# Optimization experiments

Hardware: AMD Instinct MI355X
Metric: run time of the kernel (lower is better)

Reference implementation:

```python
import jax, jax.numpy as jnp
import numpy as np

N, E, H, EC, K, NH = 50000, 640000, 128, 64, 128, 4
Hh, Kh = H // NH, K // NH
LOG2 = float(np.log(2.0))

def ssp(x):
    # ShiftedSoftplus: softplus(x) - log(2)
    return jax.nn.softplus(x) - LOG2

def ln(x, g, b, eps=1e-5):
    m = jnp.mean(x, axis=-1, keepdims=True)
    v = jnp.var(x, axis=-1, keepdims=True)
    return (x - m) * jax.lax.rsqrt(v + eps) * g + b

def setup_inputs() -> dict:
    key = jax.random.key(0)
    ks = jax.random.split(key, 24)
    def nrm(k, shape, scale):
        return jax.random.normal(k, shape, jnp.float32) * scale
    s_h = 1.0 / np.sqrt(Hh); s_e = 1.0 / np.sqrt(EC); s_k = 1.0 / np.sqrt(Kh)
    inp = {}
    inp['x'] = nrm(ks[0], (N, H), 1.0)
    inp['edge_attr'] = nrm(ks[1], (E, EC), 1.0)
    inp['edge_index'] = jax.random.randint(ks[2], (2, E), 0, N)
    # grouped Conv1d(H,K,1,groups=NH) == per-head linear: weight (NH, Kh, Hh)
    inp['k_w'] = nrm(ks[3], (NH, Kh, Hh), s_h)
    inp['q_w'] = nrm(ks[4], (NH, Kh, Hh), s_h)
    inp['v_w'] = nrm(ks[5], (NH, Hh, Hh), s_h)
    inp['wk1_w'] = nrm(ks[6], (Kh, EC), s_e); inp['wk1_b'] = nrm(ks[7], (Kh,), 0.01)
    inp['wk2_w'] = nrm(ks[8], (Kh, Kh), s_k); inp['wk2_b'] = nrm(ks[9], (Kh,), 0.01)
    inp['wkl_w'] = nrm(ks[10], (Kh, Kh), s_k); inp['wkl_b'] = nrm(ks[11], (Kh,), 0.01)
    inp['wv1_w'] = nrm(ks[12], (Hh, EC), s_e); inp['wv1_b'] = nrm(ks[13], (Hh,), 0.01)
    inp['wv2_w'] = nrm(ks[14], (Hh, Hh), s_h); inp['wv2_b'] = nrm(ks[15], (Hh,), 0.01)
    inp['wvl_w'] = nrm(ks[16], (Hh, Hh), s_h); inp['wvl_b'] = nrm(ks[17], (Hh,), 0.01)
    inp['out_w'] = nrm(ks[18], (H, H), 1.0 / np.sqrt(H)); inp['out_b'] = nrm(ks[19], (H,), 0.01)
    inp['ln1_g'] = jnp.ones((H,), jnp.float32); inp['ln1_b'] = jnp.zeros((H,), jnp.float32)
    inp['ln2_g'] = jnp.ones((H,), jnp.float32); inp['ln2_b'] = jnp.zeros((H,), jnp.float32)
    return inp

def reference(x, edge_attr, k_w, q_w, v_w, wk1_w, wk1_b, wk2_w, wk2_b, wkl_w, wkl_b,
              wv1_w, wv1_b, wv2_w, wv2_b, wvl_w, wvl_b, out_w, out_b,
              ln1_g, ln1_b, ln2_g, ln2_b, edge_index):
    row, col = edge_index[0], edge_index[1]
    y = ln(x, ln1_g, ln1_b)
    yh = y.reshape(N, NH, Hh)
    h_k = jnp.einsum('nhd,hkd->nhk', yh, k_w)  # (N,NH,Kh)
    h_q = jnp.einsum('nhd,hkd->nhk', yh, q_w)
    h_v = jnp.einsum('nhd,hkd->nhk', yh, v_w)  # (N,NH,Hh)
    Wk = ssp(edge_attr @ wk1_w.T + wk1_b) @ wk2_w.T + wk2_b  # (E,Kh)
    keys_j = jnp.einsum('ehk,jk->ehj', Wk[:, None, :] * h_k[col], wkl_w) + wkl_b
    qk = jnp.sum(h_q[row] * keys_j, axis=-1)  # (E,NH)
    # scatter softmax over destination node `row`
    m = jax.ops.segment_max(qk, row, num_segments=N)
    ex = jnp.exp(qk - m[row])
    denom = jax.ops.segment_sum(ex, row, num_segments=N)
    alpha = ex / denom[row]  # (E,NH)
    Wv = ssp(edge_attr @ wv1_w.T + wv1_b) @ wv2_w.T + wv2_b  # (E,Hh)
    msg = jnp.einsum('ehd,jd->ehj', Wv[:, None, :] * h_v[col], wvl_w) + wvl_b
    msg = alpha[..., None] * msg  # (E,NH,Hh)
    aggr = jax.ops.segment_sum(msg, row, num_segments=N).reshape(N, H)
    x2 = aggr + x
    y2 = ln(x2, ln2_g, ln2_b)
    return ssp(y2) @ out_w.T + out_b + x2
```

## Files before the change

### kernel.cpp

```cpp
#include <hip/hip_runtime.h>
#include <math.h>

#define NN 50000
#define EE 640000
#define HD 128
#define ECD 64
#define NHD 4
#define HH 32
#define SCAN_B 256
#define NBLK ((NN + SCAN_B - 1) / SCAN_B)
#define LSTR 33
#define NTILE ((NN + 15) / 16)

typedef short bf16x8 __attribute__((ext_vector_type(8)));
typedef float f32x4 __attribute__((ext_vector_type(4)));

__device__ __forceinline__ float ssp_f(float v) {
    return fmaxf(v, 0.0f) + __logf(1.0f + __expf(-fabsf(v))) - 0.69314718055994531f;
}
__device__ __forceinline__ unsigned f2bf_u(float f) {
    unsigned u = __float_as_uint(f);
    unsigned r = ((u >> 16) & 1u) + 0x7FFFu;
    return (u + r) >> 16;
}
__device__ __forceinline__ unsigned pk2(float a, float b) {
    return f2bf_u(a) | (f2bf_u(b) << 16);
}
__device__ __forceinline__ unsigned f2bf_f(float f) {
    return (__float_as_uint(f) + 0x8000u) >> 16;
}
__device__ __forceinline__ unsigned pk2f(float a, float b) {
    return f2bf_f(a) | (f2bf_f(b) << 16);
}
__device__ __forceinline__ void unp2(unsigned u, float& a, float& b) {
    a = __uint_as_float(u << 16);
    b = __uint_as_float(u & 0xffff0000u);
}
__device__ __forceinline__ bf16x8 as_bf(uint4 u) {
    union { uint4 a; bf16x8 b; } c; c.a = u; return c.b;
}

__global__ __launch_bounds__(256) void k_ln1(
    const float* __restrict__ x, const float* __restrict__ ln1_g,
    const float* __restrict__ ln1_b, const float* __restrict__ cw,
    unsigned* __restrict__ y_bf, float* __restrict__ c0_out)
{
    const int w = threadIdx.x >> 6, l = threadIdx.x & 63;
    const int h = l >> 4, i16 = l & 15;
    const int t0 = 2 * l;
    const float2 lg2 = *(const float2*)(ln1_g + t0);
    const float2 lb2 = *(const float2*)(ln1_b + t0);
    const float2 cw2 = *(const float2*)(cw + t0);

    for (int n = blockIdx.x * 4 + w; n < NN; n += 2048 * 4) {
        const float2 xv = *(const float2*)(x + (size_t)n * HD + t0);
        float s1 = xv.x + xv.y;
        float s2 = xv.x * xv.x + xv.y * xv.y;
        #pragma unroll
        for (int off = 1; off < 64; off <<= 1) {
            s1 += __shfl_xor(s1, off);
            s2 += __shfl_xor(s2, off);
        }
        const float mean = s1 * (1.0f / HD);
        const float var  = s2 * (1.0f / HD) - mean * mean;
        const float rstd = rsqrtf(var + 1e-5f);
        const float y0 = (xv.x - mean) * rstd * lg2.x + lb2.x;
        const float y1 = (xv.y - mean) * rstd * lg2.y + lb2.y;
        y_bf[(size_t)n * 64 + l] = pk2(y0, y1);

        float p = y0 * cw2.x + y1 * cw2.y;
        #pragma unroll
        for (int off = 1; off < 16; off <<= 1) p += __shfl_xor(p, off);
        if (i16 == 0) c0_out[n * NHD + h] = p;
    }
}

__global__ __launch_bounds__(256) void k_pwfrag(
    const float* __restrict__ kw, const float* __restrict__ vw,
    const float* __restrict__ qw, const float* __restrict__ wklw,
    const float* __restrict__ wklb,
    uint4* __restrict__ pf, float* __restrict__ cw)
{
    const int t = threadIdx.x;
    #pragma unroll
    for (int it = 0; it < 6; ++it) {
        const int f = t + it * 256;
        const int tg = f >> 9;
        const int rem = f & 511;
        const int nt = rem >> 6, l = rem & 63;
        const int lm = l & 15, lg = l >> 4;
        const int h = nt >> 1, od = (nt & 1) * 16 + lm;
        float val[8];
        if (tg == 2) {
            #pragma unroll
            for (int j = 0; j < 8; ++j) {
                float s = 0.f;
                for (int j2 = 0; j2 < 32; ++j2)
                    s += qw[(size_t)(h * 32 + j2) * 32 + lg * 8 + j] * wklw[j2 * 32 + od];
                val[j] = s;
            }
        } else {
            const float* wp = (tg == 0) ? kw : vw;
            #pragma unroll
            for (int j = 0; j < 8; ++j)
                val[j] = wp[(size_t)(h * 32 + od) * 32 + lg * 8 + j];
        }
        uint4 o;
        o.x = pk2(val[0], val[1]); o.y = pk2(val[2], val[3]);
        o.z = pk2(val[4], val[5]); o.w = pk2(val[6], val[7]);
        pf[f] = o;
    }
    #pragma unroll
    for (int d2 = 0; d2 < 2; ++d2) {
        const int idx = t * 2 + d2;
        const int h = idx >> 5, d = idx & 31;
        float s = 0.f;
        for (int j = 0; j < 32; ++j)
            s += qw[(size_t)(h * 32 + j) * 32 + d] * wklb[j];
        cw[idx] = s;
    }
}

__global__ __launch_bounds__(256) void k_proj(
    const unsigned* __restrict__ y_bf, const uint4* __restrict__ pf,
    unsigned short* __restrict__ hk16, unsigned short* __restrict__ hv16,
    unsigned short* __restrict__ g16)
{
    const int w = threadIdx.x >> 6, l = threadIdx.x & 63;
    const int lm = l & 15, lg = l >> 4;
    const int tile = blockIdx.x * 4 + w;
    if (tile >= NTILE) return;
    const int n0 = tile * 16;

    uint4 af[4];
    #pragma unroll
    for (int h = 0; h < 4; ++h)
        af[h] = *(const uint4*)(y_bf + (size_t)(n0 + lm) * 64 + h * 16 + lg * 4);

    unsigned short* const outs[3] = {hk16, hv16, g16};
    #pragma unroll
    for (int tg = 0; tg < 3; ++tg) {
        f32x4 acc[8];
        #pragma unroll
        for (int nt = 0; nt < 8; ++nt) {
            acc[nt] = f32x4{0.f, 0.f, 0.f, 0.f};
            acc[nt] = __builtin_amdgcn_mfma_f32_16x16x32_bf16(
                as_bf(af[nt >> 1]), as_bf(pf[tg * 512 + nt * 64 + l]), acc[nt], 0, 0, 0);
        }
        unsigned short* o = outs[tg];
        #pragma unroll
        for (int nt = 0; nt < 8; ++nt)
            #pragma unroll
            for (int r = 0; r < 4; ++r)
                o[(size_t)(n0 + lg * 4 + r) * HD + nt * 16 + lm] =
                    (unsigned short)f2bf_u(acc[nt][r]);
    }
}

__global__ __launch_bounds__(256) void k_deg(
    const int* __restrict__ edge_index, int* __restrict__ deg)
{
    for (int e = blockIdx.x * blockDim.x + threadIdx.x; e < EE;
         e += gridDim.x * blockDim.x)
        atomicAdd(&deg[edge_index[e]], 1);
}

__global__ __launch_bounds__(SCAN_B) void k_scan_block(
    const int* __restrict__ deg, int* __restrict__ base, int* __restrict__ bsum)
{
    const int i = blockIdx.x * SCAN_B + threadIdx.x;
    const int v = (i < NN) ? deg[i] : 0;
    __shared__ int s[SCAN_B];
    s[threadIdx.x] = v;
    __syncthreads();
    for (int off = 1; off < SCAN_B; off <<= 1) {
        int t = (threadIdx.x >= off) ? s[threadIdx.x - off] : 0;
        __syncthreads();
        s[threadIdx.x] += t;
        __syncthreads();
    }
    if (i < NN) base[i] = s[threadIdx.x] - v;
    if (threadIdx.x == SCAN_B - 1) bsum[blockIdx.x] = s[SCAN_B - 1];
}

__global__ __launch_bounds__(SCAN_B) void k_scan_top(int* __restrict__ bsum)
{
    const int i = threadIdx.x;
    const int v = (i < NBLK) ? bsum[i] : 0;
    __shared__ int s[SCAN_B];
    s[i] = v;
    __syncthreads();
    for (int off = 1; off < SCAN_B; off <<= 1) {
        int t = (i >= off) ? s[i - off] : 0;
        __syncthreads();
        s[i] += t;
        __syncthreads();
    }
    if (i < NBLK) bsum[i] = s[i] - v;
}

__global__ __launch_bounds__(SCAN_B) void k_scan_add(
    int* __restrict__ base, const int* __restrict__ bsum, int* __restrict__ cursor)
{
    const int i = blockIdx.x * SCAN_B + threadIdx.x;
    if (i < NN) {
        const int b = base[i] + bsum[i >> 8];
        base[i] = b;
        cursor[i] = b;
    }
}

__global__ __launch_bounds__(256) void k_scatter(
    const int* __restrict__ edge_index, int* __restrict__ cursor,
    int* __restrict__ eidx, int* __restrict__ rowv, int* __restrict__ colv)
{
    for (int e = blockIdx.x * blockDim.x + threadIdx.x; e < EE;
         e += gridDim.x * blockDim.x) {
        const int r = edge_index[e];
        const int pos = atomicAdd(&cursor[r], 1);
        eidx[pos] = e;
        rowv[pos] = r;
        colv[pos] = edge_index[EE + e];
    }
}

__global__ __launch_bounds__(256) void k_ea_csr(
    const float* __restrict__ ea, const int* __restrict__ eidx,
    unsigned* __restrict__ ea_bf)
{
    for (int i = blockIdx.x * 256 + threadIdx.x; i < EE * 32;
         i += 2048 * 256) {
        const int pos = i >> 5, u = i & 31;
        const int e = eidx[pos];
        const float2 v = *(const float2*)(ea + (size_t)e * ECD + u * 2);
        ea_bf[(size_t)pos * 32 + u] = pk2(v.x, v.y);
    }
}

__global__ __launch_bounds__(256) void k_wfrag(
    const float* __restrict__ wk1_w, const float* __restrict__ wk2_w,
    const float* __restrict__ wv1_w, const float* __restrict__ wv2_w,
    uint4* __restrict__ frag)
{
    const int t = threadIdx.x;
    const int l = t & 63;
    const int lm = l & 15, lg = l >> 4;
    {
        const int f = t >> 6;
        const int kt = f >> 1, nt = f & 1;
        const int out = nt * 16 + lm;
        uint4 a, b;
        unsigned ra[4], rb[4];
        #pragma unroll
        for (int p = 0; p < 4; ++p) {
            const int in0 = kt * 32 + lg * 8 + 2 * p;
            ra[p] = pk2(wk1_w[(size_t)out * ECD + in0], wk1_w[(size_t)out * ECD + in0 + 1]);
            rb[p] = pk2(wv1_w[(size_t)out * ECD + in0], wv1_w[(size_t)out * ECD + in0 + 1]);
        }
        a.x = ra[0]; a.y = ra[1]; a.z = ra[2]; a.w = ra[3];
        b.x = rb[0]; b.y = rb[1]; b.z = rb[2]; b.w = rb[3];
        frag[f * 64 + l] = a;
        frag[(6 + f) * 64 + l] = b;
    }
    if (t < 128) {
        const int nt = t >> 6;
        const int out = nt * 16 + lm;
        uint4 a, b;
        unsigned ra[4], rb[4];
        #pragma unroll
        for (int p = 0; p < 4; ++p) {
            const int in0 = lg * 8 + 2 * p;
            ra[p] = pk2(wk2_w[(size_t)out * HH + in0], wk2_w[(size_t)out * HH + in0 + 1]);
            rb[p] = pk2(wv2_w[(size_t)out * HH + in0], wv2_w[(size_t)out * HH + in0 + 1]);
        }
        a.x = ra[0]; a.y = ra[1]; a.z = ra[2]; a.w = ra[3];
        b.x = rb[0]; b.y = rb[1]; b.z = rb[2]; b.w = rb[3];
        frag[(4 + nt) * 64 + l] = a;
        frag[(10 + nt) * 64 + l] = b;
    }
}

__global__ __launch_bounds__(256) void k_owfrag(
    const float* __restrict__ out_w, uint4* __restrict__ owf)
{
    const int t = threadIdx.x;
    const int l = t & 63;
    const int lm = l & 15, lg = l >> 4;
    #pragma unroll
    for (int it = 0; it < 8; ++it) {
        const int f = (t >> 6) + it * 4;
        const int nt = f >> 2, kt = f & 3;
        const int n = nt * 16 + lm;
        unsigned r[4];
        #pragma unroll
        for (int p = 0; p < 4; ++p) {
            const int k0 = kt * 32 + lg * 8 + 2 * p;
            r[p] = pk2(out_w[(size_t)n * HD + k0], out_w[(size_t)n * HD + k0 + 1]);
        }
        uint4 o; o.x = r[0]; o.y = r[1]; o.z = r[2]; o.w = r[3];
        owf[f * 64 + l] = o;
    }
}

__global__ __launch_bounds__(256) void k_edge_mfma(
    const unsigned* __restrict__ ea_bf,
    const int* __restrict__ rowv, const int* __restrict__ colv,
    const unsigned* __restrict__ hk_bf, const unsigned* __restrict__ g_bf,
    const float* __restrict__ c0_in, const uint4* __restrict__ frag,
    const float* __restrict__ wk1_b, const float* __restrict__ wk2_b,
    const float* __restrict__ wv1_b, const float* __restrict__ wv2_b,
    float* __restrict__ qkP, unsigned* __restrict__ wvP)
{
    __shared__ float lds[4][64 * LSTR];
    const int w = threadIdx.x >> 6, l = threadIdx.x & 63;
    const int lm = l & 15, lg = l >> 4;
    float* L = lds[w];
    const int e0 = blockIdx.x * 256 + w * 64;
    const int pos = e0 + l;
    const int row = rowv[pos];
    const int col = colv[pos];

    uint4 eaf[4][2];
    #pragma unroll
    for (int mt = 0; mt < 4; ++mt)
        #pragma unroll
        for (int kt = 0; kt < 2; ++kt)
            eaf[mt][kt] = *(const uint4*)(ea_bf +
                (size_t)(e0 + mt * 16 + lm) * 32 + kt * 16 + lg * 4);

    {
        const float b1a = wk1_b[lm], b1b = wk1_b[16 + lm];
        f32x4 acc[4][2];
        #pragma unroll
        for (int mt = 0; mt < 4; ++mt) {
            acc[mt][0] = f32x4{b1a, b1a, b1a, b1a};
            acc[mt][1] = f32x4{b1b, b1b, b1b, b1b};
        }
        const uint4 f00 = frag[0 * 64 + l], f01 = frag[1 * 64 + l];
        const uint4 f10 = frag[2 * 64 + l], f11 = frag[3 * 64 + l];
        #pragma unroll
        for (int mt = 0; mt < 4; ++mt) {
            acc[mt][0] = __builtin_amdgcn_mfma_f32_16x16x32_bf16(as_bf(eaf[mt][0]), as_bf(f00), acc[mt][0], 0, 0, 0);
            acc[mt][1] = __builtin_amdgcn_mfma_f32_16x16x32_bf16(as_bf(eaf[mt][0]), as_bf(f01), acc[mt][1], 0, 0, 0);
            acc[mt][0] = __builtin_amdgcn_mfma_f32_16x16x32_bf16(as_bf(eaf[mt][1]), as_bf(f10), acc[mt][0], 0, 0, 0);
            acc[mt][1] = __builtin_amdgcn_mfma_f32_16x16x32_bf16(as_bf(eaf[mt][1]), as_bf(f11), acc[mt][1], 0, 0, 0);
        }
        #pragma unroll
        for (int mt = 0; mt < 4; ++mt)
            #pragma unroll
            for (int nt = 0; nt < 2; ++nt)
                #pragma unroll
                for (int r = 0; r < 4; ++r)
                    L[(mt * 16 + lg * 4 + r) * LSTR + nt * 16 + lm] = ssp_f(acc[mt][nt][r]);

        const float b2a = wk2_b[lm], b2b = wk2_b[16 + lm];
        f32x4 acc2[4][2];
        const uint4 f20 = frag[4 * 64 + l], f21 = frag[5 * 64 + l];
        #pragma unroll
        for (int mt = 0; mt < 4; ++mt) {
            acc2[mt][0] = f32x4{b2a, b2a, b2a, b2a};
            acc2[mt][1] = f32x4{b2b, b2b, b2b, b2b};
            float av[8];
            #pragma unroll
            for (int j = 0; j < 8; ++j)
                av[j] = L[(mt * 16 + lm) * LSTR + lg * 8 + j];
            uint4 a2;
            a2.x = pk2f(av[0], av[1]); a2.y = pk2f(av[2], av[3]);
            a2.z = pk2f(av[4], av[5]); a2.w = pk2f(av[6], av[7]);
            acc2[mt][0] = __builtin_amdgcn_mfma_f32_16x16x32_bf16(as_bf(a2), as_bf(f20), acc2[mt][0], 0, 0, 0);
            acc2[mt][1] = __builtin_amdgcn_mfma_f32_16x16x32_bf16(as_bf(a2), as_bf(f21), acc2[mt][1], 0, 0, 0);
        }
        #pragma unroll
        for (int mt = 0; mt < 4; ++mt)
            #pragma unroll
            for (int nt = 0; nt < 2; ++nt)
                #pragma unroll
                for (int r = 0; r < 4; ++r)
                    L[(mt * 16 + lg * 4 + r) * LSTR + nt * 16 + lm] = acc2[mt][nt][r];
    }

    float wk[32];
    #pragma unroll
    for (int j = 0; j < 32; ++j) wk[j] = L[l * LSTR + j];

    {
        const uint4* hkp = (const uint4*)(hk_bf + (size_t)col * 64);
        const uint4* gp  = (const uint4*)(g_bf  + (size_t)row * 64);
        const float4 c0v = *(const float4*)(c0_in + (size_t)row * NHD);
        #pragma unroll
        for (int h = 0; h < NHD; ++h) {
            float s = 0.f;
            #pragma unroll
            for (int q = 0; q < 4; ++q) {
                const uint4 ku = hkp[h * 4 + q];
                const uint4 gu = gp[h * 4 + q];
                float ka, kb, ga, gb;
                unp2(ku.x, ka, kb); unp2(gu.x, ga, gb);
                s = fmaf(wk[q * 8 + 0] * ka, ga, s);
                s = fmaf(wk[q * 8 + 1] * kb, gb, s);
                unp2(ku.y, ka, kb); unp2(gu.y, ga, gb);
                s = fmaf(wk[q * 8 + 2] * ka, ga, s);
                s = fmaf(wk[q * 8 + 3] * kb, gb, s);
                unp2(ku.z, ka, kb); unp2(gu.z, ga, gb);
                s = fmaf(wk[q * 8 + 4] * ka, ga, s);
                s = fmaf(wk[q * 8 + 5] * kb, gb, s);
                unp2(ku.w, ka, kb); unp2(gu.w, ga, gb);
                s = fmaf(wk[q * 8 + 6] * ka, ga, s);
                s = fmaf(wk[q * 8 + 7] * kb, gb, s);
            }
            const float c0h = (h == 0) ? c0v.x : (h == 1) ? c0v.y : (h == 2) ? c0v.z : c0v.w;
            qkP[(size_t)h * EE + pos] = s + c0h;
        }
    }

    {
        const float b1a = wv1_b[lm], b1b = wv1_b[16 + lm];
        f32x4 acc[4][2];
        #pragma unroll
        for (int mt = 0; mt < 4; ++mt) {
            acc[mt][0] = f32x4{b1a, b1a, b1a, b1a};
            acc[mt][1] = f32x4{b1b, b1b, b1b, b1b};
        }
        const uint4 f00 = frag[6 * 64 + l], f01 = frag[7 * 64 + l];
        const uint4 f10 = frag[8 * 64 + l], f11 = frag[9 * 64 + l];
        #pragma unroll
        for (int mt = 0; mt < 4; ++mt) {
            acc[mt][0] = __builtin_amdgcn_mfma_f32_16x16x32_bf16(as_bf(eaf[mt][0]), as_bf(f00), acc[mt][0], 0, 0, 0);
            acc[mt][1] = __builtin_amdgcn_mfma_f32_16x16x32_bf16(as_bf(eaf[mt][0]), as_bf(f01), acc[mt][1], 0, 0, 0);
            acc[mt][0] = __builtin_amdgcn_mfma_f32_16x16x32_bf16(as_bf(eaf[mt][1]), as_bf(f10), acc[mt][0], 0, 0, 0);
            acc[mt][1] = __builtin_amdgcn_mfma_f32_16x16x32_bf16(as_bf(eaf[mt][1]), as_bf(f11), acc[mt][1], 0, 0, 0);
        }
        #pragma unroll
        for (int mt = 0; mt < 4; ++mt)
            #pragma unroll
            for (int nt = 0; nt < 2; ++nt)
                #pragma unroll
                for (int r = 0; r < 4; ++r)
                    L[(mt * 16 + lg * 4 + r) * LSTR + nt * 16 + lm] = ssp_f(acc[mt][nt][r]);

        const float b2a = wv2_b[lm], b2b = wv2_b[16 + lm];
        f32x4 acc2[4][2];
        const uint4 f20 = frag[10 * 64 + l], f21 = frag[11 * 64 + l];
        #pragma unroll
        for (int mt = 0; mt < 4; ++mt) {
            acc2[mt][0] = f32x4{b2a, b2a, b2a, b2a};
            acc2[mt][1] = f32x4{b2b, b2b, b2b, b2b};
            float av[8];
            #pragma unroll
            for (int j = 0; j < 8; ++j)
                av[j] = L[(mt * 16 + lm) * LSTR + lg * 8 + j];
            uint4 a2;
            a2.x = pk2f(av[0], av[1]); a2.y = pk2f(av[2], av[3]);
            a2.z = pk2f(av[4], av[5]); a2.w = pk2f(av[6], av[7]);
            acc2[mt][0] = __builtin_amdgcn_mfma_f32_16x16x32_bf16(as_bf(a2), as_bf(f20), acc2[mt][0], 0, 0, 0);
            acc2[mt][1] = __builtin_amdgcn_mfma_f32_16x16x32_bf16(as_bf(a2), as_bf(f21), acc2[mt][1], 0, 0, 0);
        }
        #pragma unroll
        for (int mt = 0; mt < 4; ++mt)
            #pragma unroll
            for (int nt = 0; nt < 2; ++nt)
                #pragma unroll
                for (int r = 0; r < 4; ++r)
                    L[(mt * 16 + lg * 4 + r) * LSTR + nt * 16 + lm] = acc2[mt][nt][r];
    }

    #pragma unroll
    for (int k = 0; k < 16; ++k) {
        const int f = k * 64 + l;
        const int pr = f >> 4, i = f & 15;
        wvP[(size_t)e0 * 16 + f] = pk2f(L[pr * LSTR + 2 * i], L[pr * LSTR + 2 * i + 1]);
    }
}

__global__ __launch_bounds__(256) void k_aggr_tail(
    const float* __restrict__ qkP, const unsigned* __restrict__ wvP,
    const unsigned* __restrict__ hv_bf, const int* __restrict__ colv,
    const int* __restrict__ base, const int* __restrict__ deg,
    const float* __restrict__ x,
    const float* __restrict__ wvl_w, const float* __restrict__ wvl_b,
    const float* __restrict__ ln2_g, const float* __restrict__ ln2_b,
    float* __restrict__ x2P, unsigned* __restrict__ sbf)
{
    __shared__ float swvl[HH * 34];
    __shared__ float su[4][HD];
    for (int idx = threadIdx.x; idx < HH * HH; idx += 256)
        swvl[(idx >> 5) * 34 + (idx & 31)] = wvl_w[idx];
    __syncthreads();

    const int w = threadIdx.x >> 6, l = threadIdx.x & 63;
    const int h = l >> 4, i = l & 15;
    const int t0 = 2 * l;
    const float2 lg2 = *(const float2*)(ln2_g + t0);
    const float2 lb2 = *(const float2*)(ln2_b + t0);
    const int j0 = 2 * i;
    const float2 wb2 = *(const float2*)(wvl_b + j0);
    float* sb = su[w];

    for (int n = blockIdx.x * 4 + w; n < NN; n += 2048 * 4) {
        const int b0 = base[n];
        const int dn = deg[n];
        const float2 xv = *(const float2*)(x + (size_t)n * HD + t0);

        float acc0 = 0.f, acc1 = 0.f;
        if (dn > 0) {
            const float* qkh = qkP + (size_t)h * EE + b0;
            const int emax = b0 + dn - 1;
            float m = -3.0e38f;
            for (int c = i; c < dn; c += 16) m = fmaxf(m, qkh[c]);
            #pragma unroll
            for (int off = 1; off < 16; off <<= 1)
                m = fmaxf(m, __shfl_xor(m, off));
            float den = 0.f;
            for (int c = i; c < dn; c += 16) den += __expf(qkh[c] - m);
            #pragma unroll
            for (int off = 1; off < 16; off <<= 1) den += __shfl_xor(den, off);
            const float rden = (den > 0.f) ? 1.0f / den : 0.f;
            for (int c0 = 0; c0 < dn; c0 += 16) {
                const int tn = (dn - c0 < 16) ? (dn - c0) : 16;
                float ex = 0.f; int cq = 0;
                if (i < tn) {
                    ex = __expf(qkh[c0 + i] - m) * rden;
                    cq = colv[b0 + c0 + i];
                }
                const int t4 = (tn + 3) & ~3;
                for (int i2 = 0; i2 < t4; i2 += 4) {
                    #pragma unroll
                    for (int u = 0; u < 4; ++u) {
                        const int src = (l & 48) | (i2 + u);
                        const float wgt = __shfl(ex, src);
                        const int ce = __shfl(cq, src);
                        int ep = b0 + c0 + i2 + u;
                        ep = (ep > emax) ? emax : ep;
                        const unsigned hvv = hv_bf[(size_t)ce * 64 + l];
                        const unsigned wvv = wvP[(size_t)ep * 16 + i];
                        float ha, hb, wa, wb;
                        unp2(hvv, ha, hb); unp2(wvv, wa, wb);
                        acc0 = fmaf(wgt, wa * ha, acc0);
                        acc1 = fmaf(wgt, wb * hb, acc1);
                    }
                }
            }
        }

        *(float2*)(sb + t0) = make_float2(acc0, acc1);

        float ag0 = 0.f, ag1 = 0.f;
        if (dn > 0) {
            ag0 = wb2.x; ag1 = wb2.y;
            const float* uh = sb + h * HH;
            const float* r0 = swvl + j0 * 34;
            const float* r1 = r0 + 34;
            #pragma unroll
            for (int q = 0; q < 16; ++q) {
                const float2 u  = *(const float2*)(uh + 2 * q);
                const float2 a  = *(const float2*)(r0 + 2 * q);
                const float2 bb = *(const float2*)(r1 + 2 * q);
                ag0 = fmaf(u.x, a.x, ag0);  ag0 = fmaf(u.y, a.y, ag0);
                ag1 = fmaf(u.x, bb.x, ag1); ag1 = fmaf(u.y, bb.y, ag1);
            }
        }
        const float x20 = ag0 + xv.x;
        const float x21 = ag1 + xv.y;

        float s1 = x20 + x21, s2 = x20 * x20 + x21 * x21;
        #pragma unroll
        for (int off = 1; off < 64; off <<= 1) {
            s1 += __shfl_xor(s1, off);
            s2 += __shfl_xor(s2, off);
        }
        const float mean = s1 * (1.0f / HD);
        const float var  = s2 * (1.0f / HD) - mean * mean;
        const float rstd = rsqrtf(var + 1e-5f);
        const float ss0 = ssp_f((x20 - mean) * rstd * lg2.x + lb2.x);
        const float ss1 = ssp_f((x21 - mean) * rstd * lg2.y + lb2.y);

        *(float2*)(x2P + (size_t)n * HD + t0) = make_float2(x20, x21);
        sbf[(size_t)n * 64 + l] = pk2(ss0, ss1);
    }
}

__global__ __launch_bounds__(256) void k_tail_gemm(
    const unsigned short* __restrict__ sbf, const float* __restrict__ x2P,
    const uint4* __restrict__ owf, const float* __restrict__ out_b,
    float* __restrict__ out)
{
    const int w = threadIdx.x >> 6, l = threadIdx.x & 63;
    const int lm = l & 15, lg = l >> 4;
    const int tile = blockIdx.x * 4 + w;
    if (tile * 16 >= NN) return;
    const int n0 = tile * 16;

    uint4 af[4];
    #pragma unroll
    for (int kt = 0; kt < 4; ++kt)
        af[kt] = *(const uint4*)(sbf + (size_t)(n0 + lm) * HD + kt * 32 + lg * 8);

    f32x4 acc[8];
    #pragma unroll
    for (int nt = 0; nt < 8; ++nt) {
        const float b = out_b[nt * 16 + lm];
        acc[nt] = f32x4{b, b, b, b};
    }
    #pragma unroll
    for (int kt = 0; kt < 4; ++kt) {
        #pragma unroll
        for (int nt = 0; nt < 8; ++nt)
            acc[nt] = __builtin_amdgcn_mfma_f32_16x16x32_bf16(
                as_bf(af[kt]), as_bf(owf[(nt * 4 + kt) * 64 + l]), acc[nt], 0, 0, 0);
    }
    #pragma unroll
    for (int nt = 0; nt < 8; ++nt)
        #pragma unroll
        for (int r = 0; r < 4; ++r) {
            const size_t idx = (size_t)(n0 + lg * 4 + r) * HD + nt * 16 + lm;
            out[idx] = acc[nt][r] + x2P[idx];
        }
}

extern "C" void kernel_launch(void* const* d_in, const int* in_sizes, int n_in,
                              void* d_out, int out_size, void* d_ws, size_t ws_size,
                              hipStream_t stream) {
    const float* x         = (const float*)d_in[0];
    const float* edge_attr = (const float*)d_in[1];
    const int*   edge_index= (const int*)  d_in[2];
    const float* k_w   = (const float*)d_in[3];
    const float* q_w   = (const float*)d_in[4];
    const float* v_w   = (const float*)d_in[5];
    const float* wk1_w = (const float*)d_in[6];
    const float* wk1_b = (const float*)d_in[7];
    const float* wk2_w = (const float*)d_in[8];
    const float* wk2_b = (const float*)d_in[9];
    const float* wkl_w = (const float*)d_in[10];
    const float* wkl_b = (const float*)d_in[11];
    const float* wv1_w = (const float*)d_in[12];
    const float* wv1_b = (const float*)d_in[13];
    const float* wv2_w = (const float*)d_in[14];
    const float* wv2_b = (const float*)d_in[15];
    const float* wvl_w = (const float*)d_in[16];
    const float* wvl_b = (const float*)d_in[17];
    const float* out_w = (const float*)d_in[18];
    const float* out_b = (const float*)d_in[19];
    const float* ln1_g = (const float*)d_in[20];
    const float* ln1_b = (const float*)d_in[21];
    const float* ln2_g = (const float*)d_in[22];
    const float* ln2_b = (const float*)d_in[23];

    char* ws = (char*)d_ws;
    unsigned* hk_bf = (unsigned*)ws;            ws += (size_t)NN * 64 * 4;
    unsigned* hv_bf = (unsigned*)ws;            ws += (size_t)NN * 64 * 4;
    unsigned* g_bf  = (unsigned*)ws;            ws += (size_t)NN * 64 * 4;
    unsigned* y_bf  = (unsigned*)ws;            ws += (size_t)NN * 64 * 4;
    float* c0  = (float*)ws;                    ws += (size_t)NN * NHD * 4;
    float* qkP = (float*)ws;                    ws += (size_t)NHD * EE * 4;
    unsigned* wvP = (unsigned*)ws;              ws += (size_t)EE * 16 * 4;
    unsigned* ea_bf = (unsigned*)ws;            ws += (size_t)EE * 32 * 4;
    uint4* fragbuf = (uint4*)ws;                ws += (size_t)12 * 64 * 16;
    uint4* owfbuf  = (uint4*)ws;                ws += (size_t)32 * 64 * 16;
    uint4* pfbuf   = (uint4*)ws;                ws += (size_t)3 * 512 * 16;
    float* cw      = (float*)ws;                ws += (size_t)512 * 4;
    float* x2P = (float*)ws;                    ws += (size_t)NN * HD * 4;
    unsigned* sbf = (unsigned*)ws;              ws += (size_t)NN * 64 * 4;
    int* deg    = (int*)ws;                     ws += (size_t)NN * 4;
    int* base   = (int*)ws;                     ws += (size_t)NN * 4;
    int* cursor = (int*)ws;                     ws += (size_t)NN * 4;
    int* bsum   = (int*)ws;                     ws += (size_t)SCAN_B * 4;
    int* eidx   = (int*)ws;                     ws += (size_t)EE * 4;
    int* rowv   = (int*)ws;                     ws += (size_t)EE * 4;
    int* colv   = (int*)ws;                     ws += (size_t)EE * 4;

    (void)hipMemsetAsync(deg, 0, (size_t)NN * 4, stream);

    k_wfrag<<<1, 256, 0, stream>>>(wk1_w, wk2_w, wv1_w, wv2_w, fragbuf);
    k_owfrag<<<1, 256, 0, stream>>>(out_w, owfbuf);
    k_pwfrag<<<1, 256, 0, stream>>>(k_w, v_w, q_w, wkl_w, wkl_b, pfbuf, cw);
    k_ln1<<<2048, 256, 0, stream>>>(x, ln1_g, ln1_b, cw, y_bf, c0);
    k_proj<<<(NTILE + 3) / 4, 256, 0, stream>>>(y_bf, pfbuf,
        (unsigned short*)hk_bf, (unsigned short*)hv_bf, (unsigned short*)g_bf);
    k_deg<<<1024, 256, 0, stream>>>(edge_index, deg);
    k_scan_block<<<NBLK, SCAN_B, 0, stream>>>(deg, base, bsum);
    k_scan_top<<<1, SCAN_B, 0, stream>>>(bsum);
    k_scan_add<<<NBLK, SCAN_B, 0, stream>>>(base, bsum, cursor);
    k_scatter<<<1024, 256, 0, stream>>>(edge_index, cursor, eidx, rowv, colv);
    k_ea_csr<<<2048, 256, 0, stream>>>(edge_attr, eidx, ea_bf);
    k_edge_mfma<<<EE / 256, 256, 0, stream>>>(ea_bf, rowv, colv,
        hk_bf, g_bf, c0, fragbuf,
        wk1_b, wk2_b, wv1_b, wv2_b, qkP, wvP);
    k_aggr_tail<<<2048, 256, 0, stream>>>(qkP, wvP, hv_bf, colv, base, deg,
        x, wvl_w, wvl_b, ln2_g, ln2_b, x2P, sbf);
    k_tail_gemm<<<(NN / 16 + 3) / 4, 256, 0, stream>>>(
        (const unsigned short*)sbf, x2P, owfbuf, out_b, (float*)d_out);
}
```

Measured before the change: 361.4 us.

## Fuse LayerNorm into projection GEMM and gather edge_attr directly in edge kernel

```diff
diff --git a/kernel.cpp b/kernel.cpp
--- a/kernel.cpp
+++ b/kernel.cpp
@@ -10,7 +10,7 @@
 #define SCAN_B 256
 #define NBLK ((NN + SCAN_B - 1) / SCAN_B)
 #define LSTR 33
-#define NTILE ((NN + 15) / 16)
+#define NTILE (NN / 16)
 
 typedef short bf16x8 __attribute__((ext_vector_type(8)));
 typedef float f32x4 __attribute__((ext_vector_type(4)));
@@ -38,41 +38,6 @@
 }
 __device__ __forceinline__ bf16x8 as_bf(uint4 u) {
     union { uint4 a; bf16x8 b; } c; c.a = u; return c.b;
-}
-
-__global__ __launch_bounds__(256) void k_ln1(
-    const float* __restrict__ x, const float* __restrict__ ln1_g,
-    const float* __restrict__ ln1_b, const float* __restrict__ cw,
-    unsigned* __restrict__ y_bf, float* __restrict__ c0_out)
-{
-    const int w = threadIdx.x >> 6, l = threadIdx.x & 63;
-    const int h = l >> 4, i16 = l & 15;
-    const int t0 = 2 * l;
-    const float2 lg2 = *(const float2*)(ln1_g + t0);
-    const float2 lb2 = *(const float2*)(ln1_b + t0);
-    const float2 cw2 = *(const float2*)(cw + t0);
-
-    for (int n = blockIdx.x * 4 + w; n < NN; n += 2048 * 4) {
-        const float2 xv = *(const float2*)(x + (size_t)n * HD + t0);
-        float s1 = xv.x + xv.y;
-        float s2 = xv.x * xv.x + xv.y * xv.y;
-        #pragma unroll
-        for (int off = 1; off < 64; off <<= 1) {
-            s1 += __shfl_xor(s1, off);
-            s2 += __shfl_xor(s2, off);
-        }
-        const float mean = s1 * (1.0f / HD);
-        const float var  = s2 * (1.0f / HD) - mean * mean;
-        const float rstd = rsqrtf(var + 1e-5f);
-        const float y0 = (xv.x - mean) * rstd * lg2.x + lb2.x;
-        const float y1 = (xv.y - mean) * rstd * lg2.y + lb2.y;
-        y_bf[(size_t)n * 64 + l] = pk2(y0, y1);
-
-        float p = y0 * cw2.x + y1 * cw2.y;
-        #pragma unroll
-        for (int off = 1; off < 16; off <<= 1) p += __shfl_xor(p, off);
-        if (i16 == 0) c0_out[n * NHD + h] = p;
-    }
 }
 
 __global__ __launch_bounds__(256) void k_pwfrag(
@@ -121,39 +86,67 @@
     }
 }
 
-__global__ __launch_bounds__(256) void k_proj(
-    const unsigned* __restrict__ y_bf, const uint4* __restrict__ pf,
+__global__ __launch_bounds__(256) void k_ln1proj(
+    const float* __restrict__ x, const float* __restrict__ ln1_g,
+    const float* __restrict__ ln1_b, const float* __restrict__ cw,
+    const uint4* __restrict__ pf, float* __restrict__ c0_out,
     unsigned short* __restrict__ hk16, unsigned short* __restrict__ hv16,
     unsigned short* __restrict__ g16)
 {
+    __shared__ unsigned ylds[16][68];
     const int w = threadIdx.x >> 6, l = threadIdx.x & 63;
     const int lm = l & 15, lg = l >> 4;
-    const int tile = blockIdx.x * 4 + w;
-    if (tile >= NTILE) return;
-    const int n0 = tile * 16;
-
-    uint4 af[4];
-    #pragma unroll
-    for (int h = 0; h < 4; ++h)
-        af[h] = *(const uint4*)(y_bf + (size_t)(n0 + lm) * 64 + h * 16 + lg * 4);
-
-    unsigned short* const outs[3] = {hk16, hv16, g16};
-    #pragma unroll
-    for (int tg = 0; tg < 3; ++tg) {
-        f32x4 acc[8];
-        #pragma unroll
-        for (int nt = 0; nt < 8; ++nt) {
-            acc[nt] = f32x4{0.f, 0.f, 0.f, 0.f};
-            acc[nt] = __builtin_amdgcn_mfma_f32_16x16x32_bf16(
-                as_bf(af[nt >> 1]), as_bf(pf[tg * 512 + nt * 64 + l]), acc[nt], 0, 0, 0);
-        }
-        unsigned short* o = outs[tg];
-        #pragma unroll
-        for (int nt = 0; nt < 8; ++nt)
-            #pragma unroll
-            for (int r = 0; r < 4; ++r)
-                o[(size_t)(n0 + lg * 4 + r) * HD + nt * 16 + lm] =
-                    (unsigned short)f2bf_u(acc[nt][r]);
+    const int t0 = 2 * l;
+    const float2 lg2 = *(const float2*)(ln1_g + t0);
+    const float2 lb2 = *(const float2*)(ln1_b + t0);
+    const float2 cw2 = *(const float2*)(cw + t0);
+
+    for (int tile = blockIdx.x; tile < NTILE; tile += 1024) {
+        const int n0 = tile * 16;
+        __syncthreads();
+        #pragma unroll
+        for (int it = 0; it < 4; ++it) {
+            const int n = n0 + w * 4 + it;
+            const float2 xv = *(const float2*)(x + (size_t)n * HD + t0);
+            float s1 = xv.x + xv.y;
+            float s2 = xv.x * xv.x + xv.y * xv.y;
+            #pragma unroll
+            for (int off = 1; off < 64; off <<= 1) {
+                s1 += __shfl_xor(s1, off);
+                s2 += __shfl_xor(s2, off);
+            }
+            const float mean = s1 * (1.0f / HD);
+            const float var  = s2 * (1.0f / HD) - mean * mean;
+            const float rstd = rsqrtf(var + 1e-5f);
+            const float y0 = (xv.x - mean) * rstd * lg2.x + lb2.x;
+            const float y1 = (xv.y - mean) * rstd * lg2.y + lb2.y;
+            ylds[w * 4 + it][l] = pk2(y0, y1);
+            float p = y0 * cw2.x + y1 * cw2.y;
+            #pragma unroll
+            for (int off = 1; off < 16; off <<= 1) p += __shfl_xor(p, off);
+            if ((l & 15) == 0) c0_out[n * NHD + (l >> 4)] = p;
+        }
+        __syncthreads();
+        uint4 am;
+        am.x = ylds[lm][w * 16 + lg * 4 + 0];
+        am.y = ylds[lm][w * 16 + lg * 4 + 1];
+        am.z = ylds[lm][w * 16 + lg * 4 + 2];
+        am.w = ylds[lm][w * 16 + lg * 4 + 3];
+        #pragma unroll
+        for (int tg = 0; tg < 3; ++tg) {
+            unsigned short* o = (tg == 0) ? hk16 : (tg == 1) ? hv16 : g16;
+            #pragma unroll
+            for (int q = 0; q < 2; ++q) {
+                const int nt = 2 * w + q;
+                f32x4 acc = f32x4{0.f, 0.f, 0.f, 0.f};
+                acc = __builtin_amdgcn_mfma_f32_16x16x32_bf16(
+                    as_bf(am), as_bf(pf[tg * 512 + nt * 64 + l]), acc, 0, 0, 0);
+                #pragma unroll
+                for (int r = 0; r < 4; ++r)
+                    o[(size_t)(n0 + lg * 4 + r) * HD + nt * 16 + lm] =
+                        (unsigned short)f2bf_u(acc[r]);
+            }
+        }
     }
 }
 
@@ -224,19 +217,6 @@
     }
 }
 
-__global__ __launch_bounds__(256) void k_ea_csr(
-    const float* __restrict__ ea, const int* __restrict__ eidx,
-    unsigned* __restrict__ ea_bf)
-{
-    for (int i = blockIdx.x * 256 + threadIdx.x; i < EE * 32;
-         i += 2048 * 256) {
-        const int pos = i >> 5, u = i & 31;
-        const int e = eidx[pos];
-        const float2 v = *(const float2*)(ea + (size_t)e * ECD + u * 2);
-        ea_bf[(size_t)pos * 32 + u] = pk2(v.x, v.y);
-    }
-}
-
 __global__ __launch_bounds__(256) void k_wfrag(
     const float* __restrict__ wk1_w, const float* __restrict__ wk2_w,
     const float* __restrict__ wv1_w, const float* __restrict__ wv2_w,
@@ -303,7 +283,7 @@
 }
 
 __global__ __launch_bounds__(256) void k_edge_mfma(
-    const unsigned* __restrict__ ea_bf,
+    const float* __restrict__ ea, const int* __restrict__ eidx,
     const int* __restrict__ rowv, const int* __restrict__ colv,
     const unsigned* __restrict__ hk_bf, const unsigned* __restrict__ g_bf,
     const float* __restrict__ c0_in, const uint4* __restrict__ frag,
@@ -322,11 +302,18 @@
 
     uint4 eaf[4][2];
     #pragma unroll
-    for (int mt = 0; mt < 4; ++mt)
-        #pragma unroll
-        for (int kt = 0; kt < 2; ++kt)
-            eaf[mt][kt] = *(const uint4*)(ea_bf +
-                (size_t)(e0 + mt * 16 + lm) * 32 + kt * 16 + lg * 4);
+    for (int mt = 0; mt < 4; ++mt) {
+        const int ee = eidx[e0 + mt * 16 + lm];
+        const float* ep = ea + (size_t)ee * ECD + lg * 8;
+        const float4 a0 = *(const float4*)(ep);
+        const float4 a1 = *(const float4*)(ep + 4);
+        const float4 b0 = *(const float4*)(ep + 32);
+        const float4 b1 = *(const float4*)(ep + 36);
+        eaf[mt][0].x = pk2f(a0.x, a0.y); eaf[mt][0].y = pk2f(a0.z, a0.w);
+        eaf[mt][0].z = pk2f(a1.x, a1.y); eaf[mt][0].w = pk2f(a1.z, a1.w);
+        eaf[mt][1].x = pk2f(b0.x, b0.y); eaf[mt][1].y = pk2f(b0.z, b0.w);
+        eaf[mt][1].z = pk2f(b1.x, b1.y); eaf[mt][1].w = pk2f(b1.z, b1.w);
+    }
 
     {
         const float b1a = wk1_b[lm], b1b = wk1_b[16 + lm];
@@ -649,11 +636,9 @@
     unsigned* hk_bf = (unsigned*)ws;            ws += (size_t)NN * 64 * 4;
     unsigned* hv_bf = (unsigned*)ws;            ws += (size_t)NN * 64 * 4;
     unsigned* g_bf  = (unsigned*)ws;            ws += (size_t)NN * 64 * 4;
-    unsigned* y_bf  = (unsigned*)ws;            ws += (size_t)NN * 64 * 4;
     float* c0  = (float*)ws;                    ws += (size_t)NN * NHD * 4;
     float* qkP = (float*)ws;                    ws += (size_t)NHD * EE * 4;
     unsigned* wvP = (unsigned*)ws;              ws += (size_t)EE * 16 * 4;
-    unsigned* ea_bf = (unsigned*)ws;            ws += (size_t)EE * 32 * 4;
     uint4* fragbuf = (uint4*)ws;                ws += (size_t)12 * 64 * 16;
     uint4* owfbuf  = (uint4*)ws;                ws += (size_t)32 * 64 * 16;
     uint4* pfbuf   = (uint4*)ws;                ws += (size_t)3 * 512 * 16;
@@ -673,16 +658,14 @@
     k_wfrag<<<1, 256, 0, stream>>>(wk1_w, wk2_w, wv1_w, wv2_w, fragbuf);
     k_owfrag<<<1, 256, 0, stream>>>(out_w, owfbuf);
     k_pwfrag<<<1, 256, 0, stream>>>(k_w, v_w, q_w, wkl_w, wkl_b, pfbuf, cw);
-    k_ln1<<<2048, 256, 0, stream>>>(x, ln1_g, ln1_b, cw, y_bf, c0);
-    k_proj<<<(NTILE + 3) / 4, 256, 0, stream>>>(y_bf, pfbuf,
+    k_ln1proj<<<1024, 256, 0, stream>>>(x, ln1_g, ln1_b, cw, pfbuf, c0,
         (unsigned short*)hk_bf, (unsigned short*)hv_bf, (unsigned short*)g_bf);
     k_deg<<<1024, 256, 0, stream>>>(edge_index, deg);
     k_scan_block<<<NBLK, SCAN_B, 0, stream>>>(deg, base, bsum);
     k_scan_top<<<1, SCAN_B, 0, stream>>>(bsum);
     k_scan_add<<<NBLK, SCAN_B, 0, stream>>>(base, bsum, cursor);
     k_scatter<<<1024, 256, 0, stream>>>(edge_index, cursor, eidx, rowv, colv);
-    k_ea_csr<<<2048, 256, 0, stream>>>(edge_attr, eidx, ea_bf);
-    k_edge_mfma<<<EE / 256, 256, 0, stream>>>(ea_bf, rowv, colv,
+    k_edge_mfma<<<EE / 256, 256, 0, stream>>>(edge_attr, eidx, rowv, colv,
         hk_bf, g_bf, c0, fragbuf,
         wk1_b, wk2_b, wv1_b, wv2_b, qkP, wvP);
     k_aggr_tail<<<2048, 256, 0, stream>>>(qkP, wvP, hv_bf, colv, base, deg,
```

Result: faster. 309.4 us, median of 3 (-14.4%).
